# Optimization experiments

Measured on AMD Instinct MI355X. Metric: run time of the kernel, lower is better.

## Reference

```python
import jax, jax.numpy as jnp
import numpy as np

NEG_SLOPE = 0.2
EPS = 1e-12


def gat_conv(x, src, dst, n, W, a_src, a_dst, b):
    # x: [N, Fin]; W: [Fout, Fin]; a_src/a_dst/b: [Fout]
    h = x @ W.T                                   # [N, Fout]
    e_src = (h * a_src).sum(-1)                   # [N]
    e_dst = (h * a_dst).sum(-1)                   # [N]
    e = jax.nn.leaky_relu(e_src[src] + e_dst[dst], NEG_SLOPE)  # [E]
    m = jax.ops.segment_max(e, dst, num_segments=n)
    ex = jnp.exp(e - m[dst])
    denom = jax.ops.segment_sum(ex, dst, num_segments=n)
    alpha = ex / denom[dst]                       # scatter-softmax over in-edges
    out = jax.ops.segment_sum(alpha[:, None] * h[src], dst, num_segments=n)
    return out + b


def setup_inputs() -> dict:
    key = jax.random.key(0)
    ks = jax.random.split(key, 16)
    N, E = 50000, 800000
    Din, Dfeat, Dhid, Dout = 128, 64, 64, 32

    def lin(k, o, i):
        s = 1.0 / np.sqrt(i)
        return jax.random.uniform(k, (o, i), jnp.float32, -s, s)

    def vec(k, o, i):
        s = 1.0 / np.sqrt(i)
        return jax.random.uniform(k, (o,), jnp.float32, -s, s)

    return {
        "x": jax.random.normal(ks[0], (N, Din), jnp.float32),
        "edge_index": jax.random.randint(ks[1], (2, E), 0, N, jnp.int64),
        "W_pre": lin(ks[2], Dfeat, Din),
        "b_pre": vec(ks[3], Dfeat, Din),
        "W1": lin(ks[4], Dhid, Dfeat), "a1s": vec(ks[5], Dhid, Dhid), "a1d": vec(ks[6], Dhid, Dhid), "b1": jnp.zeros((Dhid,), jnp.float32),
        "W2": lin(ks[7], Dhid, Dhid), "a2s": vec(ks[8], Dhid, Dhid), "a2d": vec(ks[9], Dhid, Dhid), "b2": jnp.zeros((Dhid,), jnp.float32),
        "W3": lin(ks[10], Dout, Dhid), "a3s": vec(ks[11], Dout, Dout), "a3d": vec(ks[12], Dout, Dout), "b3": jnp.zeros((Dout,), jnp.float32),
    }


def reference(x, edge_index, W_pre, b_pre, W1, a1s, a1d, b1, W2, a2s, a2d, b2, W3, a3s, a3d, b3):
    n = x.shape[0]
    loops = jnp.arange(n, dtype=edge_index.dtype)
    src = jnp.concatenate([edge_index[0], loops])  # PyG add_self_loops=True
    dst = jnp.concatenate([edge_index[1], loops])

    h = x @ W_pre.T + b_pre                        # linear_pre
    h = jax.nn.relu(gat_conv(h, src, dst, n, W1, a1s, a1d, b1))
    h = jax.nn.relu(gat_conv(h, src, dst, n, W2, a2s, a2d, b2))
    h = gat_conv(h, src, dst, n, W3, a3s, a3d, b3)
    norm = jnp.maximum(jnp.linalg.norm(h, axis=-1, keepdims=True), EPS)
    return h / norm
```

## Files before the change

### kernel.cpp

```cpp
#include <hip/hip_runtime.h>
#include <hip/hip_bf16.h>
#include <math.h>

#define NEG_SLOPE 0.2f

__device__ __forceinline__ float lrelu(float x) {
    return x > 0.f ? x : NEG_SLOPE * x;
}

__device__ __forceinline__ unsigned short f32_to_bf16_rne(float v) {
    unsigned u = __float_as_uint(v);
    u = (u + 0x7FFFu + ((u >> 16) & 1u)) >> 16;
    return (unsigned short)u;
}

__device__ __forceinline__ float bf16_to_f32(unsigned short b) {
    return __uint_as_float(((unsigned)b) << 16);
}

__global__ __launch_bounds__(256)
void build_buckets_kernel(const unsigned int* __restrict__ raw, int E, int N,
                          int maxdeg, int* __restrict__ deg,
                          unsigned short* __restrict__ buckets) {
    bool is64 = true;
#pragma unroll
    for (int i = 1; i < 32; i += 2) is64 &= (raw[i] == 0u);

    const int g = blockIdx.x & 7;
    const int c = blockIdx.x >> 3;
    const int C = gridDim.x >> 3;
    const int lo = (int)(((long long)N * g) >> 3);
    const int hi = (int)(((long long)N * (g + 1)) >> 3);

    for (int e = c * 256 + (int)threadIdx.x; e < E; e += C * 256) {
        int s, d;
        if (is64) {
            s = (int)raw[2 * e];
            d = (int)raw[2 * (E + e)];
        } else {
            s = (int)raw[e];
            d = (int)raw[E + e];
        }
        if (d < lo || d >= hi) continue;
        if ((unsigned)s >= (unsigned)N) continue;
        int pos = atomicAdd(&deg[d], 1);
        if (pos < maxdeg) buckets[(size_t)d * maxdeg + pos] = (unsigned short)s;
    }
}

template <int K, int F, bool BIAS, bool ES, bool OUTB>
__global__ __launch_bounds__(256)
void transform_kernel(const float* __restrict__ X, const float* __restrict__ W,
                      const float* __restrict__ bias, const float* __restrict__ a_s,
                      const float* __restrict__ a_d, void* __restrict__ Hout,
                      float* __restrict__ es, float* __restrict__ ed, int N) {
    constexpr int FG = F / 4;
    constexpr int NG = 256 / FG;
    constexpr int NT = NG * 4;
    constexpr int KC = 64;
    constexpr int XS = NT + 4;
    constexpr int WS = F + 4;

    __shared__ float Xs[KC * XS];
    __shared__ float Wt[KC * WS];

    const int tid = threadIdx.x;
    const int ft = tid % FG;
    const int nt = tid / FG;
    const int base = blockIdx.x * NT;

    float4 acc[4];
#pragma unroll
    for (int j = 0; j < 4; ++j) acc[j] = make_float4(0.f, 0.f, 0.f, 0.f);

    for (int k0 = 0; k0 < K; k0 += KC) {
        if (k0) __syncthreads();
#pragma unroll
        for (int idx = tid; idx < F * (KC / 4); idx += 256) {
            int ff = idx / (KC / 4), kq = idx % (KC / 4);
            float4 wv = *reinterpret_cast<const float4*>(
                W + (size_t)ff * K + k0 + 4 * kq);
            Wt[(4 * kq + 0) * WS + ff] = wv.x;
            Wt[(4 * kq + 1) * WS + ff] = wv.y;
            Wt[(4 * kq + 2) * WS + ff] = wv.z;
            Wt[(4 * kq + 3) * WS + ff] = wv.w;
        }
#pragma unroll
        for (int idx = tid; idx < NT * (KC / 4); idx += 256) {
            int n = idx / (KC / 4), kq = idx % (KC / 4);
            int nn = base + n; if (nn >= N) nn = N - 1;
            float4 xv = *reinterpret_cast<const float4*>(
                X + (size_t)nn * K + k0 + 4 * kq);
            Xs[(4 * kq + 0) * XS + n] = xv.x;
            Xs[(4 * kq + 1) * XS + n] = xv.y;
            Xs[(4 * kq + 2) * XS + n] = xv.z;
            Xs[(4 * kq + 3) * XS + n] = xv.w;
        }
        __syncthreads();

#pragma unroll 4
        for (int k = 0; k < KC; ++k) {
            const float4 xv = *reinterpret_cast<const float4*>(&Xs[k * XS + 4 * nt]);
            const float4 wv = *reinterpret_cast<const float4*>(&Wt[k * WS + 4 * ft]);
            acc[0].x = fmaf(xv.x, wv.x, acc[0].x);
            acc[0].y = fmaf(xv.x, wv.y, acc[0].y);
            acc[0].z = fmaf(xv.x, wv.z, acc[0].z);
            acc[0].w = fmaf(xv.x, wv.w, acc[0].w);
            acc[1].x = fmaf(xv.y, wv.x, acc[1].x);
            acc[1].y = fmaf(xv.y, wv.y, acc[1].y);
            acc[1].z = fmaf(xv.y, wv.z, acc[1].z);
            acc[1].w = fmaf(xv.y, wv.w, acc[1].w);
            acc[2].x = fmaf(xv.z, wv.x, acc[2].x);
            acc[2].y = fmaf(xv.z, wv.y, acc[2].y);
            acc[2].z = fmaf(xv.z, wv.z, acc[2].z);
            acc[2].w = fmaf(xv.z, wv.w, acc[2].w);
            acc[3].x = fmaf(xv.w, wv.x, acc[3].x);
            acc[3].y = fmaf(xv.w, wv.y, acc[3].y);
            acc[3].z = fmaf(xv.w, wv.z, acc[3].z);
            acc[3].w = fmaf(xv.w, wv.w, acc[3].w);
        }
    }

    const int fb = 4 * ft;
    if (BIAS) {
        const float4 bv = *reinterpret_cast<const float4*>(bias + fb);
#pragma unroll
        for (int j = 0; j < 4; ++j) {
            acc[j].x += bv.x; acc[j].y += bv.y;
            acc[j].z += bv.z; acc[j].w += bv.w;
        }
    }
    const float4 av = ES ? *reinterpret_cast<const float4*>(a_s + fb)
                         : make_float4(0.f, 0.f, 0.f, 0.f);
    const float4 dv = ES ? *reinterpret_cast<const float4*>(a_d + fb)
                         : make_float4(0.f, 0.f, 0.f, 0.f);
#pragma unroll
    for (int j = 0; j < 4; ++j) {
        const int n = base + nt * 4 + j;
        if (n < N) {
            if (OUTB) {
                ushort4 o;
                o.x = f32_to_bf16_rne(acc[j].x);
                o.y = f32_to_bf16_rne(acc[j].y);
                o.z = f32_to_bf16_rne(acc[j].z);
                o.w = f32_to_bf16_rne(acc[j].w);
                *reinterpret_cast<ushort4*>(
                    (unsigned short*)Hout + (size_t)n * F + fb) = o;
            } else {
                *reinterpret_cast<float4*>(
                    (float*)Hout + (size_t)n * F + fb) = acc[j];
            }
        }
        if (ES) {
            float s = acc[j].x * av.x + acc[j].y * av.y
                    + acc[j].z * av.z + acc[j].w * av.w;
            float d = acc[j].x * dv.x + acc[j].y * dv.y
                    + acc[j].z * dv.z + acc[j].w * dv.w;
#pragma unroll
            for (int m = 1; m < FG; m <<= 1) {
                s += __shfl_xor(s, m, 64);
                d += __shfl_xor(d, m, 64);
            }
            if (ft == 0 && n < N) { es[n] = s; ed[n] = d; }
        }
    }
}

template <int F, int MODE, bool BF16IN>
__global__ __launch_bounds__(256)
void aggregate_kernel(const void* __restrict__ Hp_, const float* __restrict__ es,
                      const float* __restrict__ ed, const int* __restrict__ deg,
                      const unsigned short* __restrict__ buckets, int maxdeg,
                      const float* __restrict__ bias,
                      float* __restrict__ out, int N) {
    const float* Hpf = (const float*)Hp_;
    const unsigned short* Hpb = (const unsigned short*)Hp_;
    const int tid = threadIdx.x;
    const int lane = tid & 63;
    const int wid = tid >> 6;
    const int f = lane % F;
    const int n = blockIdx.x * 4 + wid;
    if (n >= N) return;

    int dn = deg[n];
    if (dn > maxdeg) dn = maxdeg;
    const unsigned short* bk = buckets + (size_t)n * maxdeg;
    const float edn = ed[n];

    int sv = n;
    if (lane < dn) sv = (int)bk[lane];
    float e = lrelu(es[sv] + edn);
    if (lane > dn) e = -1e30f;

    float m = e;
#pragma unroll
    for (int o = 1; o < 64; o <<= 1) m = fmaxf(m, __shfl_xor(m, o, 64));

    float ex = (lane <= dn) ? __expf(e - m) : 0.f;
    float den = ex;
#pragma unroll
    for (int o = 1; o < 64; o <<= 1) den += __shfl_xor(den, o, 64);

    const int tp = (dn + 8) & ~7;
    float a0 = 0.f, a1 = 0.f, a2 = 0.f, a3 = 0.f;
    for (int i = 0; i < tp; i += 8) {
        int   ss[8];
        float xx[8], r[8];
#pragma unroll
        for (int j = 0; j < 8; ++j) {
            ss[j] = __builtin_amdgcn_readlane(sv, i + j);
            xx[j] = __uint_as_float((unsigned)__builtin_amdgcn_readlane(
                        (int)__float_as_uint(ex), i + j));
        }
#pragma unroll
        for (int j = 0; j < 8; ++j) {
            r[j] = BF16IN ? bf16_to_f32(Hpb[(size_t)ss[j] * F + f])
                          : Hpf[(size_t)ss[j] * F + f];
        }
#pragma unroll
        for (int j = 0; j < 8; ++j) {
            if ((j & 3) == 0) a0 = fmaf(xx[j], r[j], a0);
            else if ((j & 3) == 1) a1 = fmaf(xx[j], r[j], a1);
            else if ((j & 3) == 2) a2 = fmaf(xx[j], r[j], a2);
            else a3 = fmaf(xx[j], r[j], a3);
        }
    }
    float v = ((a0 + a1) + (a2 + a3)) / den + bias[f];

    if (MODE == 0) {
        if (lane < F) out[(size_t)n * F + f] = fmaxf(v, 0.f);
    } else {
        float ss2 = v * v;
#pragma unroll
        for (int s = 1; s < F; s <<= 1) ss2 += __shfl_xor(ss2, s, 64);
        float nrm = fmaxf(sqrtf(ss2), 1e-12f);
        if (lane < F) out[(size_t)n * F + f] = v / nrm;
    }
}

extern "C" void kernel_launch(void* const* d_in, const int* in_sizes, int n_in,
                              void* d_out, int out_size, void* d_ws, size_t ws_size,
                              hipStream_t stream) {
    const float* x      = (const float*)d_in[0];
    const unsigned int* edges = (const unsigned int*)d_in[1];
    const float* W_pre  = (const float*)d_in[2];
    const float* b_pre  = (const float*)d_in[3];
    const float* W1  = (const float*)d_in[4];
    const float* a1s = (const float*)d_in[5];
    const float* a1d = (const float*)d_in[6];
    const float* b1  = (const float*)d_in[7];
    const float* W2  = (const float*)d_in[8];
    const float* a2s = (const float*)d_in[9];
    const float* a2d = (const float*)d_in[10];
    const float* b2  = (const float*)d_in[11];
    const float* W3  = (const float*)d_in[12];
    const float* a3s = (const float*)d_in[13];
    const float* a3d = (const float*)d_in[14];
    const float* b3  = (const float*)d_in[15];

    const int N = in_sizes[0] / 128;
    const int E = in_sizes[1] / 2;

    char* w = (char*)d_ws;
    size_t off = 0;
    auto alloc = [&](size_t bytes) {
        char* p = w + off;
        off = (off + bytes + 255) & ~(size_t)255;
        return p;
    };
    int*   deg = (int*)alloc((size_t)N * 4);
    float* A   = (float*)alloc((size_t)N * 64 * 4);
    float* B   = (float*)alloc((size_t)N * 64 * 4);
    unsigned short* Bb = (unsigned short*)B;
    float* es  = (float*)alloc((size_t)N * 4);
    float* ed  = (float*)alloc((size_t)N * 4);

    size_t remain = (ws_size > off) ? (ws_size - off) : 0;
    int maxdeg = (int)(remain / ((size_t)N * 2));
    if (maxdeg > 63) maxdeg = 63;
    if (maxdeg < 16) maxdeg = 16;
    unsigned short* buckets = (unsigned short*)alloc((size_t)N * (size_t)maxdeg * 2);

    hipMemsetAsync(deg, 0, (size_t)N * 4, stream);
    build_buckets_kernel<<<8 * 256, 256, 0, stream>>>(
        edges, E, N, maxdeg, deg, buckets);

    const int nb  = (N + 3) / 4;
    const int t64 = (N + 63) / 64;
    const int t32 = (N + 127) / 128;

    transform_kernel<128, 64, true, false, false><<<t64, 256, 0, stream>>>(
        x, W_pre, b_pre, nullptr, nullptr, A, nullptr, nullptr, N);

    transform_kernel<64, 64, false, true, true><<<t64, 256, 0, stream>>>(
        A, W1, nullptr, a1s, a1d, Bb, es, ed, N);
    aggregate_kernel<64, 0, true><<<nb, 256, 0, stream>>>(
        Bb, es, ed, deg, buckets, maxdeg, b1, A, N);

    transform_kernel<64, 64, false, true, true><<<t64, 256, 0, stream>>>(
        A, W2, nullptr, a2s, a2d, Bb, es, ed, N);
    aggregate_kernel<64, 0, true><<<nb, 256, 0, stream>>>(
        Bb, es, ed, deg, buckets, maxdeg, b2, A, N);

    transform_kernel<64, 32, false, true, false><<<t32, 256, 0, stream>>>(
        A, W3, nullptr, a3s, a3d, B, es, ed, N);
    aggregate_kernel<32, 1, false><<<nb, 256, 0, stream>>>(
        B, es, ed, deg, buckets, maxdeg, b3, (float*)d_out, N);
}
```

Measured before the change: 279.6 us.

## Process two nodes per wavefront in aggregation and stream X directly in transform

The aggregation kernel now assigns two destination nodes per 64-lane wavefront, with each half-wave handling one node. Each lane covers two bf16 features via a ushort2 load, and the softmax runs over two edge slots per lane. The goal is to stop idling half the lanes when F=32 and to halve the gather instruction count when F=64. The transform kernel drops the transposed X staging in shared memory and loads X rows per thread straight from global memory, keeping only the full W tile in LDS. This removes one sync and the LDS transpose, at the cost of uncoalesced per-thread row loads of X.

Result: slower. 286.5 us (+2.5%).

```diff
diff --git a/kernel.cpp b/kernel.cpp
--- a/kernel.cpp
+++ b/kernel.cpp
@@ -47,6 +47,12 @@
         if (pos < maxdeg) buckets[(size_t)d * maxdeg + pos] = (unsigned short)s;
     }
 }
+
+#define FMA4(j, xs, wv) \
+    acc[j].x = fmaf(xs, wv.x, acc[j].x); \
+    acc[j].y = fmaf(xs, wv.y, acc[j].y); \
+    acc[j].z = fmaf(xs, wv.z, acc[j].z); \
+    acc[j].w = fmaf(xs, wv.w, acc[j].w);
 
 template <int K, int F, bool BIAS, bool ES, bool OUTB>
 __global__ __launch_bounds__(256)
@@ -57,68 +63,53 @@
     constexpr int FG = F / 4;
     constexpr int NG = 256 / FG;
     constexpr int NT = NG * 4;
-    constexpr int KC = 64;
-    constexpr int XS = NT + 4;
     constexpr int WS = F + 4;
 
-    __shared__ float Xs[KC * XS];
-    __shared__ float Wt[KC * WS];
+    __shared__ float Wt[K * WS];
 
     const int tid = threadIdx.x;
     const int ft = tid % FG;
     const int nt = tid / FG;
     const int base = blockIdx.x * NT;
 
+    for (int idx = tid; idx < F * (K / 4); idx += 256) {
+        int ff = idx / (K / 4), kq = idx % (K / 4);
+        float4 wv = *reinterpret_cast<const float4*>(W + (size_t)ff * K + 4 * kq);
+        Wt[(4 * kq + 0) * WS + ff] = wv.x;
+        Wt[(4 * kq + 1) * WS + ff] = wv.y;
+        Wt[(4 * kq + 2) * WS + ff] = wv.z;
+        Wt[(4 * kq + 3) * WS + ff] = wv.w;
+    }
+    __syncthreads();
+
+    const int n0 = base + nt * 4;
+    const int c0 = (n0 + 0 < N) ? n0 + 0 : N - 1;
+    const int c1 = (n0 + 1 < N) ? n0 + 1 : N - 1;
+    const int c2 = (n0 + 2 < N) ? n0 + 2 : N - 1;
+    const int c3 = (n0 + 3 < N) ? n0 + 3 : N - 1;
+    const float* x0 = X + (size_t)c0 * K;
+    const float* x1 = X + (size_t)c1 * K;
+    const float* x2 = X + (size_t)c2 * K;
+    const float* x3 = X + (size_t)c3 * K;
+
     float4 acc[4];
 #pragma unroll
     for (int j = 0; j < 4; ++j) acc[j] = make_float4(0.f, 0.f, 0.f, 0.f);
 
-    for (int k0 = 0; k0 < K; k0 += KC) {
-        if (k0) __syncthreads();
-#pragma unroll
-        for (int idx = tid; idx < F * (KC / 4); idx += 256) {
-            int ff = idx / (KC / 4), kq = idx % (KC / 4);
-            float4 wv = *reinterpret_cast<const float4*>(
-                W + (size_t)ff * K + k0 + 4 * kq);
-            Wt[(4 * kq + 0) * WS + ff] = wv.x;
-            Wt[(4 * kq + 1) * WS + ff] = wv.y;
-            Wt[(4 * kq + 2) * WS + ff] = wv.z;
-            Wt[(4 * kq + 3) * WS + ff] = wv.w;
-        }
-#pragma unroll
-        for (int idx = tid; idx < NT * (KC / 4); idx += 256) {
-            int n = idx / (KC / 4), kq = idx % (KC / 4);
-            int nn = base + n; if (nn >= N) nn = N - 1;
-            float4 xv = *reinterpret_cast<const float4*>(
-                X + (size_t)nn * K + k0 + 4 * kq);
-            Xs[(4 * kq + 0) * XS + n] = xv.x;
-            Xs[(4 * kq + 1) * XS + n] = xv.y;
-            Xs[(4 * kq + 2) * XS + n] = xv.z;
-            Xs[(4 * kq + 3) * XS + n] = xv.w;
-        }
-        __syncthreads();
-
 #pragma unroll 4
-        for (int k = 0; k < KC; ++k) {
-            const float4 xv = *reinterpret_cast<const float4*>(&Xs[k * XS + 4 * nt]);
-            const float4 wv = *reinterpret_cast<const float4*>(&Wt[k * WS + 4 * ft]);
-            acc[0].x = fmaf(xv.x, wv.x, acc[0].x);
-            acc[0].y = fmaf(xv.x, wv.y, acc[0].y);
-            acc[0].z = fmaf(xv.x, wv.z, acc[0].z);
-            acc[0].w = fmaf(xv.x, wv.w, acc[0].w);
-            acc[1].x = fmaf(xv.y, wv.x, acc[1].x);
-            acc[1].y = fmaf(xv.y, wv.y, acc[1].y);
-            acc[1].z = fmaf(xv.y, wv.z, acc[1].z);
-            acc[1].w = fmaf(xv.y, wv.w, acc[1].w);
-            acc[2].x = fmaf(xv.z, wv.x, acc[2].x);
-            acc[2].y = fmaf(xv.z, wv.y, acc[2].y);
-            acc[2].z = fmaf(xv.z, wv.z, acc[2].z);
-            acc[2].w = fmaf(xv.z, wv.w, acc[2].w);
-            acc[3].x = fmaf(xv.w, wv.x, acc[3].x);
-            acc[3].y = fmaf(xv.w, wv.y, acc[3].y);
-            acc[3].z = fmaf(xv.w, wv.z, acc[3].z);
-            acc[3].w = fmaf(xv.w, wv.w, acc[3].w);
-        }
+    for (int kq = 0; kq < K / 4; ++kq) {
+        const float4 v0 = *reinterpret_cast<const float4*>(x0 + 4 * kq);
+        const float4 v1 = *reinterpret_cast<const float4*>(x1 + 4 * kq);
+        const float4 v2 = *reinterpret_cast<const float4*>(x2 + 4 * kq);
+        const float4 v3 = *reinterpret_cast<const float4*>(x3 + 4 * kq);
+        const float4 w0 = *reinterpret_cast<const float4*>(&Wt[(4 * kq + 0) * WS + 4 * ft]);
+        const float4 w1 = *reinterpret_cast<const float4*>(&Wt[(4 * kq + 1) * WS + 4 * ft]);
+        const float4 w2 = *reinterpret_cast<const float4*>(&Wt[(4 * kq + 2) * WS + 4 * ft]);
+        const float4 w3 = *reinterpret_cast<const float4*>(&Wt[(4 * kq + 3) * WS + 4 * ft]);
+        FMA4(0, v0.x, w0) FMA4(1, v1.x, w0) FMA4(2, v2.x, w0) FMA4(3, v3.x, w0)
+        FMA4(0, v0.y, w1) FMA4(1, v1.y, w1) FMA4(2, v2.y, w1) FMA4(3, v3.y, w1)
+        FMA4(0, v0.z, w2) FMA4(1, v1.z, w2) FMA4(2, v2.z, w2) FMA4(3, v3.z, w2)
+        FMA4(0, v0.w, w3) FMA4(1, v1.w, w3) FMA4(2, v2.w, w3) FMA4(3, v3.w, w3)
     }
 
     const int fb = 4 * ft;
@@ -136,7 +127,7 @@
                          : make_float4(0.f, 0.f, 0.f, 0.f);
 #pragma unroll
     for (int j = 0; j < 4; ++j) {
-        const int n = base + nt * 4 + j;
+        const int n = n0 + j;
         if (n < N) {
             if (OUTB) {
                 ushort4 o;
@@ -173,13 +164,15 @@
                       const unsigned short* __restrict__ buckets, int maxdeg,
                       const float* __restrict__ bias,
                       float* __restrict__ out, int N) {
+    constexpr int FPL = F / 32;
     const float* Hpf = (const float*)Hp_;
     const unsigned short* Hpb = (const unsigned short*)Hp_;
     const int tid = threadIdx.x;
     const int lane = tid & 63;
     const int wid = tid >> 6;
-    const int f = lane % F;
-    const int n = blockIdx.x * 4 + wid;
+    const int half = lane >> 5;
+    const int l32 = lane & 31;
+    const int n = blockIdx.x * 8 + wid * 2 + half;
     if (n >= N) return;
 
     int dn = deg[n];
@@ -187,54 +180,69 @@
     const unsigned short* bk = buckets + (size_t)n * maxdeg;
     const float edn = ed[n];
 
-    int sv = n;
-    if (lane < dn) sv = (int)bk[lane];
-    float e = lrelu(es[sv] + edn);
-    if (lane > dn) e = -1e30f;
-
-    float m = e;
-#pragma unroll
-    for (int o = 1; o < 64; o <<= 1) m = fmaxf(m, __shfl_xor(m, o, 64));
-
-    float ex = (lane <= dn) ? __expf(e - m) : 0.f;
-    float den = ex;
-#pragma unroll
-    for (int o = 1; o < 64; o <<= 1) den += __shfl_xor(den, o, 64);
+    const int s1i = 32 + l32;
+    int sv0 = (l32 < dn) ? (int)bk[l32] : n;
+    int sv1 = (s1i < dn) ? (int)bk[s1i] : n;
+    float e0 = lrelu(es[sv0] + edn);
+    float e1 = lrelu(es[sv1] + edn);
+    if (l32 > dn) e0 = -1e30f;
+    if (s1i > dn) e1 = -1e30f;
+
+    float m = fmaxf(e0, e1);
+#pragma unroll
+    for (int o = 1; o < 32; o <<= 1) m = fmaxf(m, __shfl_xor(m, o, 64));
+
+    float ex0 = (l32 <= dn) ? __expf(e0 - m) : 0.f;
+    float ex1 = (s1i <= dn) ? __expf(e1 - m) : 0.f;
+    float den = ex0 + ex1;
+#pragma unroll
+    for (int o = 1; o < 32; o <<= 1) den += __shfl_xor(den, o, 64);
 
     const int tp = (dn + 8) & ~7;
     float a0 = 0.f, a1 = 0.f, a2 = 0.f, a3 = 0.f;
     for (int i = 0; i < tp; i += 8) {
-        int   ss[8];
-        float xx[8], r[8];
+        const int svc = (i < 32) ? sv0 : sv1;
+        const float exc = (i < 32) ? ex0 : ex1;
+        const int jj = i & 31;
 #pragma unroll
         for (int j = 0; j < 8; ++j) {
-            ss[j] = __builtin_amdgcn_readlane(sv, i + j);
-            xx[j] = __uint_as_float((unsigned)__builtin_amdgcn_readlane(
-                        (int)__float_as_uint(ex), i + j));
-        }
-#pragma unroll
-        for (int j = 0; j < 8; ++j) {
-            r[j] = BF16IN ? bf16_to_f32(Hpb[(size_t)ss[j] * F + f])
-                          : Hpf[(size_t)ss[j] * F + f];
-        }
-#pragma unroll
-        for (int j = 0; j < 8; ++j) {
-            if ((j & 3) == 0) a0 = fmaf(xx[j], r[j], a0);
-            else if ((j & 3) == 1) a1 = fmaf(xx[j], r[j], a1);
-            else if ((j & 3) == 2) a2 = fmaf(xx[j], r[j], a2);
-            else a3 = fmaf(xx[j], r[j], a3);
-        }
-    }
-    float v = ((a0 + a1) + (a2 + a3)) / den + bias[f];
+            int sA = __builtin_amdgcn_readlane(svc, jj + j);
+            int sB = __builtin_amdgcn_readlane(svc, 32 + jj + j);
+            int xA = __builtin_amdgcn_readlane((int)__float_as_uint(exc), jj + j);
+            int xB = __builtin_amdgcn_readlane((int)__float_as_uint(exc), 32 + jj + j);
+            const int   ss = half ? sB : sA;
+            const float xx = __uint_as_float((unsigned)(half ? xB : xA));
+            if (FPL == 2) {
+                ushort2 rv = *reinterpret_cast<const ushort2*>(
+                    Hpb + (size_t)ss * F + 2 * l32);
+                float r0 = bf16_to_f32(rv.x), r1 = bf16_to_f32(rv.y);
+                if (j & 1) { a1 = fmaf(xx, r0, a1); a3 = fmaf(xx, r1, a3); }
+                else       { a0 = fmaf(xx, r0, a0); a2 = fmaf(xx, r1, a2); }
+            } else {
+                float r = Hpf[(size_t)ss * F + l32];
+                if ((j & 3) == 0) a0 = fmaf(xx, r, a0);
+                else if ((j & 3) == 1) a1 = fmaf(xx, r, a1);
+                else if ((j & 3) == 2) a2 = fmaf(xx, r, a2);
+                else a3 = fmaf(xx, r, a3);
+            }
+        }
+    }
 
     if (MODE == 0) {
-        if (lane < F) out[(size_t)n * F + f] = fmaxf(v, 0.f);
+        const float2 bv = *reinterpret_cast<const float2*>(bias + 2 * l32);
+        float v0 = (a0 + a1) / den + bv.x;
+        float v1 = (a2 + a3) / den + bv.y;
+        float2 o;
+        o.x = fmaxf(v0, 0.f);
+        o.y = fmaxf(v1, 0.f);
+        *reinterpret_cast<float2*>(out + (size_t)n * F + 2 * l32) = o;
     } else {
+        float v = ((a0 + a1) + (a2 + a3)) / den + bias[l32];
         float ss2 = v * v;
 #pragma unroll
-        for (int s = 1; s < F; s <<= 1) ss2 += __shfl_xor(ss2, s, 64);
+        for (int o = 1; o < 32; o <<= 1) ss2 += __shfl_xor(ss2, o, 64);
         float nrm = fmaxf(sqrtf(ss2), 1e-12f);
-        if (lane < F) out[(size_t)n * F + f] = v / nrm;
+        out[(size_t)n * F + l32] = v / nrm;
     }
 }
 
@@ -285,7 +293,7 @@
     build_buckets_kernel<<<8 * 256, 256, 0, stream>>>(
         edges, E, N, maxdeg, deg, buckets);
 
-    const int nb  = (N + 3) / 4;
+    const int nb  = (N + 7) / 8;
     const int t64 = (N + 63) / 64;
     const int t32 = (N + 127) / 128;
 
```
